# Kernel optimization log

Hardware: AMD Instinct MI355X
Metric: run time of the kernel (lower is better)

## Reference

```python
import jax, jax.numpy as jnp
import numpy as np

KH, KW = 3, 3
PAD, STRIDE, DIL, GROUPS = 1, 1, 1, 1
KK = KH * KW


def setup_inputs() -> dict:
    key = jax.random.key(0)
    ks = jax.random.split(key, 5)
    B, Cin, H, W = 8, 256, 64, 64
    Cout = 256
    x = jax.random.normal(ks[0], (B, Cin, H, W), jnp.float32)
    # offset conv: Conv2d(Cin -> 2*KK, 3x3, pad 1), small init so offsets are modest
    w_off = jax.random.normal(ks[1], (2 * KK, Cin, KH, KW), jnp.float32) * 0.01
    b_off = jax.random.normal(ks[2], (2 * KK,), jnp.float32) * 0.01
    # deformable conv weights: [Cout, Cin/groups, KH, KW]
    w_dcn = jax.random.normal(ks[3], (Cout, Cin // GROUPS, KH, KW), jnp.float32) * 0.05
    b_dcn = jax.random.normal(ks[4], (Cout,), jnp.float32) * 0.05
    return {"x": x, "w_off": w_off, "b_off": b_off, "w_dcn": w_dcn, "b_dcn": b_dcn}


def _deform_conv2d(x, offsets, w, b):
    """Deformable conv v1 (torchvision semantics, zero padding outside image).
    x: [B,Cin,Hin,Win], offsets: [B,2*KK,Ho,Wo] with (dy,dx) interleaved per tap.
    """
    B, Cin, Hin, Win = x.shape
    Ho, Wo = offsets.shape[2], offsets.shape[3]
    Cout = w.shape[0]

    off = offsets.reshape(B, KK, 2, Ho, Wo)
    off_y, off_x = off[:, :, 0], off[:, :, 1]  # [B,KK,Ho,Wo]

    # base sampling grid per kernel tap k = kh*KW + kw
    base_ky = (jnp.repeat(jnp.arange(KH), KW) * DIL).astype(jnp.float32)  # [KK]
    base_kx = (jnp.tile(jnp.arange(KW), KH) * DIL).astype(jnp.float32)
    hs = (jnp.arange(Ho) * STRIDE - PAD).astype(jnp.float32)
    ws = (jnp.arange(Wo) * STRIDE - PAD).astype(jnp.float32)

    py = hs[None, None, :, None] + base_ky[None, :, None, None] + off_y  # [B,KK,Ho,Wo]
    px = ws[None, None, None, :] + base_kx[None, :, None, None] + off_x

    iy0f = jnp.floor(py)
    ix0f = jnp.floor(px)
    fy = py - iy0f
    fx = px - ix0f
    iy0 = iy0f.astype(jnp.int32)
    ix0 = ix0f.astype(jnp.int32)

    x_flat = x.reshape(B, Cin, Hin * Win)

    def gather(iy, ix, wgt):
        valid = (iy >= 0) & (iy < Hin) & (ix >= 0) & (ix < Win)
        idx = (jnp.clip(iy, 0, Hin - 1) * Win + jnp.clip(ix, 0, Win - 1)).reshape(B, -1)
        vals = jnp.take_along_axis(x_flat, idx[:, None, :], axis=2)  # [B,Cin,KK*Ho*Wo]
        return vals * (wgt * valid).reshape(B, 1, -1)

    samp = (gather(iy0, ix0, (1 - fy) * (1 - fx))
            + gather(iy0, ix0 + 1, (1 - fy) * fx)
            + gather(iy0 + 1, ix0, fy * (1 - fx))
            + gather(iy0 + 1, ix0 + 1, fy * fx))  # [B,Cin,KK*Ho*Wo]

    samp = samp.reshape(B, GROUPS, Cin // GROUPS, KK, Ho, Wo)
    wg = w.reshape(GROUPS, Cout // GROUPS, Cin // GROUPS, KK)
    out = jnp.einsum('gock,bgckhw->bgohw', wg, samp).reshape(B, Cout, Ho, Wo)
    return out + b[None, :, None, None]


def reference(x, w_off, b_off, w_dcn, b_dcn):
    offsets = jax.lax.conv_general_dilated(
        x, w_off, window_strides=(STRIDE, STRIDE),
        padding=[(PAD, PAD), (PAD, PAD)], rhs_dilation=(DIL, DIL),
        dimension_numbers=('NCHW', 'OIHW', 'NCHW')) + b_off[None, :, None, None]
    return _deform_conv2d(x, offsets, w_dcn, b_dcn)
```

## Files before the change

### kernel.cpp

```cpp
#include <hip/hip_runtime.h>

#define HN 64
#define WN 64
#define HW 4096
#define CIN 256
#define COUT 256
#define NKK 9
#define OFFC 18
#define KTOT 2304
#define CICH 32
#define KCH 288
#define SROW 296
#define NCHUNK 8

typedef __attribute__((ext_vector_type(8))) short bf16x8;
typedef __attribute__((ext_vector_type(4))) float f32x4;

static __device__ __forceinline__ unsigned short f2bf(float f) {
    unsigned u = __float_as_uint(f);
    return (unsigned short)((u + 0x7FFFu + ((u >> 16) & 1u)) >> 16);
}
static __device__ __forceinline__ unsigned pk2(float a, float b) {
    return (unsigned)f2bf(a) | ((unsigned)f2bf(b) << 16);
}
static __device__ __forceinline__ float bf2f(short s) {
    return __uint_as_float(((unsigned)(unsigned short)s) << 16);
}

__global__ __launch_bounds__(256) void prep_kernel(
    const float* __restrict__ x, const float* __restrict__ w_dcn,
    const float* __restrict__ w_off, unsigned short* __restrict__ xh,
    unsigned short* __restrict__ wd_b, unsigned short* __restrict__ wo_b)
{
    const int blk = blockIdx.x;
    const int t = threadIdx.x;
    if (blk < 512) {
        __shared__ unsigned short lds[64 * 264];
        const int b = blk >> 6;
        const int row = blk & 63;
        const int p = t & 63;
        const int cb = (t >> 6) * 8;
        const float* xp = x + (size_t)b * CIN * HW + row * WN + p;
#pragma unroll
        for (int i = 0; i < 8; ++i) {
            const int c0 = cb + i * 32;
            float v[8];
#pragma unroll
            for (int j = 0; j < 8; ++j)
                v[j] = xp[(size_t)(c0 + j) * HW];
            uint4 o = { pk2(v[0],v[1]), pk2(v[2],v[3]), pk2(v[4],v[5]), pk2(v[6],v[7]) };
            *(uint4*)&lds[p * 264 + c0] = o;
        }
        __syncthreads();
        unsigned short* op = xh + ((size_t)b * HW + row * WN) * CIN;
#pragma unroll
        for (int i = 0; i < 8; ++i) {
            const int idx = i * 256 + t;
            const int cg = idx & 31, pp = idx >> 5;
            *(uint4*)(op + (size_t)pp * CIN + cg * 8) = *(const uint4*)&lds[pp * 264 + cg * 8];
        }
    } else if (blk < 768) {
        const int cout = blk - 512;
        for (int id = t; id < 288; id += 256) {
            const int k = id * 8;
            const int kk = k >> 8, c0 = k & 255;
            const float* wp = w_dcn + (size_t)cout * KTOT + kk;
            float v[8];
#pragma unroll
            for (int j = 0; j < 8; ++j) v[j] = wp[(size_t)(c0 + j) * NKK];
            uint4 o = { pk2(v[0],v[1]), pk2(v[2],v[3]), pk2(v[4],v[5]), pk2(v[6],v[7]) };
            *(uint4*)(wd_b + (size_t)cout * KTOT + k) = o;
        }
    } else {
        const int r = blk - 768;
        for (int id = t; id < 288; id += 256) {
            const int k = id * 8;
            const int kk = k >> 8, c0 = k & 255;
            uint4 o = {0u, 0u, 0u, 0u};
            if (r < OFFC) {
                const float* wp = w_off + (size_t)r * KTOT + kk;
                float v[8];
#pragma unroll
                for (int j = 0; j < 8; ++j) v[j] = wp[(size_t)(c0 + j) * NKK];
                o = (uint4){ pk2(v[0],v[1]), pk2(v[2],v[3]), pk2(v[4],v[5]), pk2(v[6],v[7]) };
            }
            *(uint4*)(wo_b + (size_t)r * KTOT + k) = o;
        }
    }
}

__global__ __launch_bounds__(256) void offs_mfma_kernel(
    const unsigned short* __restrict__ xh, const unsigned short* __restrict__ wo_b,
    const float* __restrict__ b_off, float* __restrict__ offs)
{
    __shared__ unsigned short samp[64 * SROW];
    const int blk = blockIdx.x;
    const int b = blk >> 6;
    const int tile = blk & 63;
    const int ty0 = (tile >> 3) << 3;
    const int tx0 = (tile & 7) << 3;
    const int t = threadIdx.x;
    const int lane = t & 63;
    const int wave = t >> 6;
    const unsigned short* xb = xh + (size_t)b * HW * CIN;

    f32x4 acc0 = {0.f,0.f,0.f,0.f}, acc1 = {0.f,0.f,0.f,0.f};

    for (int chunk = 0; chunk < NCHUNK; ++chunk) {
        const int ci0 = chunk * CICH;
        __syncthreads();
        for (int id = t; id < 2304; id += 256) {
            const int kk = id >> 8;
            const int px = (id >> 2) & 63;
            const int g = id & 3;
            const int ky = kk / 3;
            const int oy = ty0 + (px >> 3) + ky - 1;
            const int ox = tx0 + (px & 7) + (kk - ky * 3) - 1;
            bf16x8 v = {0,0,0,0,0,0,0,0};
            if ((unsigned)oy < HN && (unsigned)ox < WN)
                v = *(const bf16x8*)(xb + (size_t)(oy * WN + ox) * CIN + ci0 + g * 8);
            *(bf16x8*)&samp[px * SROW + kk * 32 + g * 8] = v;
        }
        __syncthreads();
        const unsigned short* wb = wo_b + (size_t)(lane & 15) * KTOT + ci0 + (lane >> 4) * 8;
        const unsigned short* sb = &samp[(wave * 16 + (lane & 15)) * SROW + (lane >> 4) * 8];
#pragma unroll
        for (int s = 0; s < 9; ++s) {
            const bf16x8 bfr = *(const bf16x8*)(sb + s * 32);
            const bf16x8 a0 = *(const bf16x8*)(wb + s * 256);
            const bf16x8 a1 = *(const bf16x8*)(wb + (size_t)16 * KTOT + s * 256);
            acc0 = __builtin_amdgcn_mfma_f32_16x16x32_bf16(a0, bfr, acc0, 0, 0, 0);
            acc1 = __builtin_amdgcn_mfma_f32_16x16x32_bf16(a1, bfr, acc1, 0, 0, 0);
        }
    }
    const int px = wave * 16 + (lane & 15);
    const int wy = ty0 + (px >> 3), wx = tx0 + (px & 7);
#pragma unroll
    for (int j = 0; j < 4; ++j) {
        const int c0 = (lane >> 4) * 4 + j;
        if (c0 < OFFC)
            offs[((size_t)b * OFFC + c0) * HW + wy * WN + wx] = acc0[j] + b_off[c0];
        const int c1 = 16 + c0;
        if (c1 < OFFC)
            offs[((size_t)b * OFFC + c1) * HW + wy * WN + wx] = acc1[j] + b_off[c1];
    }
}

__global__ __launch_bounds__(512, 4) void dcn_mfma_kernel(
    const unsigned short* __restrict__ xh, const float* __restrict__ offs,
    const unsigned short* __restrict__ wd_b, const float* __restrict__ bias,
    float* __restrict__ out)
{
    __shared__ unsigned short samp[64 * SROW];
    __shared__ uint4  tidx[576];
    __shared__ float4 twgt[576];

    const int blk = blockIdx.x;
    const int b = blk >> 6;
    const int tile = blk & 63;
    const int ty0 = (tile >> 3) << 3;
    const int tx0 = (tile & 7) << 3;
    const int t = threadIdx.x;
    const int lane = t & 63;
    const int wave = t >> 6;
    const unsigned short* xb = xh + (size_t)b * HW * CIN;

    for (int i = t; i < 576; i += 512) {
        const int kk = i >> 6, p = i & 63;
        const int oy = ty0 + (p >> 3), ox = tx0 + (p & 7);
        const float offy = offs[((size_t)b * OFFC + 2 * kk) * HW + oy * WN + ox];
        const float offx = offs[((size_t)b * OFFC + 2 * kk + 1) * HW + oy * WN + ox];
        const int ky = kk / 3;
        const float pyf = (float)(oy - 1 + ky) + offy;
        const float pxf = (float)(ox - 1 + (kk - ky * 3)) + offx;
        const float fy0 = floorf(pyf), fx0 = floorf(pxf);
        const int iy0 = (int)fy0, ix0 = (int)fx0;
        const int iy1 = iy0 + 1, ix1 = ix0 + 1;
        const float fy = pyf - fy0, fx = pxf - fx0;
        const float vy0 = ((unsigned)iy0 < HN) ? 1.f : 0.f;
        const float vy1 = ((unsigned)iy1 < HN) ? 1.f : 0.f;
        const float vx0 = ((unsigned)ix0 < WN) ? 1.f : 0.f;
        const float vx1 = ((unsigned)ix1 < WN) ? 1.f : 0.f;
        const int cy0 = min(max(iy0, 0), HN - 1), cy1 = min(max(iy1, 0), HN - 1);
        const int cx0 = min(max(ix0, 0), WN - 1), cx1 = min(max(ix1, 0), WN - 1);
        tidx[i] = make_uint4((unsigned)(cy0 * WN + cx0) * CIN, (unsigned)(cy0 * WN + cx1) * CIN,
                             (unsigned)(cy1 * WN + cx0) * CIN, (unsigned)(cy1 * WN + cx1) * CIN);
        twgt[i] = make_float4((1.f - fy) * (1.f - fx) * vy0 * vx0,
                              (1.f - fy) * fx * vy0 * vx1,
                              fy * (1.f - fx) * vy1 * vx0,
                              fy * fx * vy1 * vx1);
    }

    f32x4 acc[2][4];
#pragma unroll
    for (int i = 0; i < 2; ++i)
#pragma unroll
        for (int j = 0; j < 4; ++j) acc[i][j] = (f32x4){0.f, 0.f, 0.f, 0.f};

    for (int chunk = 0; chunk < NCHUNK; ++chunk) {
        const int ci0 = chunk * CICH;
        __syncthreads();
        for (int id = t; id < 2304; id += 512) {
            const int kk = id >> 8;
            const int px = (id >> 2) & 63;
            const int g = id & 3;
            const uint4 ti = tidx[kk * 64 + px];
            const float4 tw = twgt[kk * 64 + px];
            const unsigned short* base = xb + ci0 + g * 8;
            const bf16x8 A  = *(const bf16x8*)(base + ti.x);
            const bf16x8 Bv = *(const bf16x8*)(base + ti.y);
            const bf16x8 Cv = *(const bf16x8*)(base + ti.z);
            const bf16x8 Dv = *(const bf16x8*)(base + ti.w);
            unsigned r[4];
#pragma unroll
            for (int q = 0; q < 4; ++q) {
                const float v0 = tw.x * bf2f(A[2*q])   + tw.y * bf2f(Bv[2*q])
                               + tw.z * bf2f(Cv[2*q])  + tw.w * bf2f(Dv[2*q]);
                const float v1 = tw.x * bf2f(A[2*q+1]) + tw.y * bf2f(Bv[2*q+1])
                               + tw.z * bf2f(Cv[2*q+1])+ tw.w * bf2f(Dv[2*q+1]);
                r[q] = pk2(v0, v1);
            }
            *(uint4*)&samp[px * SROW + kk * 32 + g * 8] = (uint4){r[0], r[1], r[2], r[3]};
        }
        __syncthreads();
        const unsigned short* wb = wd_b + (size_t)(wave * 32 + (lane & 15)) * KTOT + ci0 + (lane >> 4) * 8;
        const unsigned short* sb = &samp[(lane & 15) * SROW + (lane >> 4) * 8];
#pragma unroll
        for (int s = 0; s < 9; ++s) {
            bf16x8 afr[2], bfr[4];
            afr[0] = *(const bf16x8*)(wb + s * 256);
            afr[1] = *(const bf16x8*)(wb + (size_t)16 * KTOT + s * 256);
#pragma unroll
            for (int pt = 0; pt < 4; ++pt)
                bfr[pt] = *(const bf16x8*)(sb + pt * 16 * SROW + s * 32);
#pragma unroll
            for (int ct = 0; ct < 2; ++ct)
#pragma unroll
                for (int pt = 0; pt < 4; ++pt)
                    acc[ct][pt] = __builtin_amdgcn_mfma_f32_16x16x32_bf16(afr[ct], bfr[pt], acc[ct][pt], 0, 0, 0);
        }
    }

#pragma unroll
    for (int ct = 0; ct < 2; ++ct) {
#pragma unroll
        for (int pt = 0; pt < 4; ++pt) {
            const int px = pt * 16 + (lane & 15);
            const int wy = ty0 + (px >> 3), wx = tx0 + (px & 7);
#pragma unroll
            for (int j = 0; j < 4; ++j) {
                const int cout = wave * 32 + ct * 16 + (lane >> 4) * 4 + j;
                out[((size_t)b * COUT + cout) * HW + wy * WN + wx] = acc[ct][pt][j] + bias[cout];
            }
        }
    }
}

extern "C" void kernel_launch(void* const* d_in, const int* in_sizes, int n_in,
                              void* d_out, int out_size, void* d_ws, size_t ws_size,
                              hipStream_t stream) {
    const float* x     = (const float*)d_in[0];
    const float* w_off = (const float*)d_in[1];
    const float* b_off = (const float*)d_in[2];
    const float* w_dcn = (const float*)d_in[3];
    const float* b_dcn = (const float*)d_in[4];
    float* out = (float*)d_out;

    float* offs          = (float*)d_ws;
    unsigned short* wd_b = (unsigned short*)((char*)d_ws + 2359296);
    unsigned short* wo_b = (unsigned short*)((char*)d_ws + 2359296 + 1179648);
    unsigned short* xh   = (unsigned short*)((char*)d_ws + 2359296 + 1179648 + 147456);

    prep_kernel<<<800, 256, 0, stream>>>(x, w_dcn, w_off, xh, wd_b, wo_b);
    offs_mfma_kernel<<<512, 256, 0, stream>>>(xh, wo_b, b_off, offs);
    dcn_mfma_kernel<<<512, 512, 0, stream>>>(xh, offs, wd_b, b_dcn, out);
}
```

Measured before the change: 235.4 us.

## Drop LDS staging in offset conv, widen DCN blocks to 1024 threads

The offset-conv kernel stops staging im2col tiles in shared memory. Each lane now loads its bf16 fragments straight from global memory, which removes the barriers and LDS traffic. The deformable conv kernel moves to 1024-thread blocks, so each wave owns 16 output channels instead of 32. This halves per-wave accumulators and spreads the bilinear sampling across more threads. Block-to-(batch, tile) mapping is interleaved across batches, and the sampling loads are split to reduce register pressure, at the cost of fewer MFMAs per A-fragment and redundant global reads in the offset kernel.

```diff
diff --git a/kernel.cpp b/kernel.cpp
--- a/kernel.cpp
+++ b/kernel.cpp
@@ -93,48 +93,40 @@
     const unsigned short* __restrict__ xh, const unsigned short* __restrict__ wo_b,
     const float* __restrict__ b_off, float* __restrict__ offs)
 {
-    __shared__ unsigned short samp[64 * SROW];
     const int blk = blockIdx.x;
-    const int b = blk >> 6;
-    const int tile = blk & 63;
+    const int b = blk & 7;
+    const int tile = blk >> 3;
     const int ty0 = (tile >> 3) << 3;
     const int tx0 = (tile & 7) << 3;
     const int t = threadIdx.x;
     const int lane = t & 63;
     const int wave = t >> 6;
-    const unsigned short* xb = xh + (size_t)b * HW * CIN;
+    const int pxl = wave * 16 + (lane & 15);
+    const int kq8 = (lane >> 4) * 8;
+    const int oy = ty0 + (pxl >> 3);
+    const int ox = tx0 + (pxl & 7);
+    const unsigned short* xb = xh + (size_t)b * HW * CIN + kq8;
+    const unsigned short* wrow = wo_b + (size_t)(lane & 15) * KTOT + kq8;
 
     f32x4 acc0 = {0.f,0.f,0.f,0.f}, acc1 = {0.f,0.f,0.f,0.f};
-
-    for (int chunk = 0; chunk < NCHUNK; ++chunk) {
-        const int ci0 = chunk * CICH;
-        __syncthreads();
-        for (int id = t; id < 2304; id += 256) {
-            const int kk = id >> 8;
-            const int px = (id >> 2) & 63;
-            const int g = id & 3;
-            const int ky = kk / 3;
-            const int oy = ty0 + (px >> 3) + ky - 1;
-            const int ox = tx0 + (px & 7) + (kk - ky * 3) - 1;
-            bf16x8 v = {0,0,0,0,0,0,0,0};
-            if ((unsigned)oy < HN && (unsigned)ox < WN)
-                v = *(const bf16x8*)(xb + (size_t)(oy * WN + ox) * CIN + ci0 + g * 8);
-            *(bf16x8*)&samp[px * SROW + kk * 32 + g * 8] = v;
-        }
-        __syncthreads();
-        const unsigned short* wb = wo_b + (size_t)(lane & 15) * KTOT + ci0 + (lane >> 4) * 8;
-        const unsigned short* sb = &samp[(wave * 16 + (lane & 15)) * SROW + (lane >> 4) * 8];
-#pragma unroll
-        for (int s = 0; s < 9; ++s) {
-            const bf16x8 bfr = *(const bf16x8*)(sb + s * 32);
-            const bf16x8 a0 = *(const bf16x8*)(wb + s * 256);
-            const bf16x8 a1 = *(const bf16x8*)(wb + (size_t)16 * KTOT + s * 256);
+#pragma unroll
+    for (int kk = 0; kk < 9; ++kk) {
+        const int yy = oy + kk / 3 - 1;
+        const int xx = ox + kk % 3 - 1;
+        const bool valid = ((unsigned)yy < HN) && ((unsigned)xx < WN);
+        const unsigned short* bp = xb + (size_t)(yy * WN + xx) * CIN;
+        const unsigned short* wp = wrow + kk * 256;
+#pragma unroll
+        for (int s = 0; s < 8; ++s) {
+            const bf16x8 bfr = valid ? *(const bf16x8*)(bp + s * 32)
+                                     : (bf16x8){0,0,0,0,0,0,0,0};
+            const bf16x8 a0 = *(const bf16x8*)(wp + s * 32);
+            const bf16x8 a1 = *(const bf16x8*)(wp + (size_t)16 * KTOT + s * 32);
             acc0 = __builtin_amdgcn_mfma_f32_16x16x32_bf16(a0, bfr, acc0, 0, 0, 0);
             acc1 = __builtin_amdgcn_mfma_f32_16x16x32_bf16(a1, bfr, acc1, 0, 0, 0);
         }
     }
-    const int px = wave * 16 + (lane & 15);
-    const int wy = ty0 + (px >> 3), wx = tx0 + (px & 7);
+    const int wy = ty0 + (pxl >> 3), wx = tx0 + (pxl & 7);
 #pragma unroll
     for (int j = 0; j < 4; ++j) {
         const int c0 = (lane >> 4) * 4 + j;
@@ -146,7 +138,31 @@
     }
 }
 
-__global__ __launch_bounds__(512, 4) void dcn_mfma_kernel(
+static __device__ __forceinline__ void sample_one(
+    int id, const unsigned short* __restrict__ xb, int ci0,
+    const uint4* __restrict__ tidx, const float4* __restrict__ twgt,
+    unsigned short* __restrict__ samp)
+{
+    const int kk = id >> 8;
+    const int px = (id >> 2) & 63;
+    const int g  = id & 3;
+    const uint4  ti = tidx[kk * 64 + px];
+    const float4 tw = twgt[kk * 64 + px];
+    const unsigned short* base = xb + ci0 + g * 8;
+    const bf16x8 A  = *(const bf16x8*)(base + ti.x);
+    const bf16x8 Bv = *(const bf16x8*)(base + ti.y);
+    float v[8];
+#pragma unroll
+    for (int e = 0; e < 8; ++e) v[e] = tw.x * bf2f(A[e]) + tw.y * bf2f(Bv[e]);
+    const bf16x8 Cv = *(const bf16x8*)(base + ti.z);
+    const bf16x8 Dv = *(const bf16x8*)(base + ti.w);
+#pragma unroll
+    for (int e = 0; e < 8; ++e) v[e] += tw.z * bf2f(Cv[e]) + tw.w * bf2f(Dv[e]);
+    uint4 o = { pk2(v[0],v[1]), pk2(v[2],v[3]), pk2(v[4],v[5]), pk2(v[6],v[7]) };
+    *(uint4*)&samp[px * SROW + kk * 32 + g * 8] = o;
+}
+
+__global__ __launch_bounds__(1024, 8) void dcn_mfma_kernel(
     const unsigned short* __restrict__ xh, const float* __restrict__ offs,
     const unsigned short* __restrict__ wd_b, const float* __restrict__ bias,
     float* __restrict__ out)
@@ -156,8 +172,8 @@
     __shared__ float4 twgt[576];
 
     const int blk = blockIdx.x;
-    const int b = blk >> 6;
-    const int tile = blk & 63;
+    const int b = blk & 7;
+    const int tile = blk >> 3;
     const int ty0 = (tile >> 3) << 3;
     const int tx0 = (tile & 7) << 3;
     const int t = threadIdx.x;
@@ -165,7 +181,7 @@
     const int wave = t >> 6;
     const unsigned short* xb = xh + (size_t)b * HW * CIN;
 
-    for (int i = t; i < 576; i += 512) {
+    for (int i = t; i < 576; i += 1024) {
         const int kk = i >> 6, p = i & 63;
         const int oy = ty0 + (p >> 3), ox = tx0 + (p & 7);
         const float offy = offs[((size_t)b * OFFC + 2 * kk) * HW + oy * WN + ox];
@@ -191,68 +207,46 @@
                               fy * fx * vy1 * vx1);
     }
 
-    f32x4 acc[2][4];
-#pragma unroll
-    for (int i = 0; i < 2; ++i)
-#pragma unroll
-        for (int j = 0; j < 4; ++j) acc[i][j] = (f32x4){0.f, 0.f, 0.f, 0.f};
+    f32x4 acc0 = {0.f,0.f,0.f,0.f}, acc1 = {0.f,0.f,0.f,0.f};
+    f32x4 acc2 = {0.f,0.f,0.f,0.f}, acc3 = {0.f,0.f,0.f,0.f};
 
     for (int chunk = 0; chunk < NCHUNK; ++chunk) {
         const int ci0 = chunk * CICH;
         __syncthreads();
-        for (int id = t; id < 2304; id += 512) {
-            const int kk = id >> 8;
-            const int px = (id >> 2) & 63;
-            const int g = id & 3;
-            const uint4 ti = tidx[kk * 64 + px];
-            const float4 tw = twgt[kk * 64 + px];
-            const unsigned short* base = xb + ci0 + g * 8;
-            const bf16x8 A  = *(const bf16x8*)(base + ti.x);
-            const bf16x8 Bv = *(const bf16x8*)(base + ti.y);
-            const bf16x8 Cv = *(const bf16x8*)(base + ti.z);
-            const bf16x8 Dv = *(const bf16x8*)(base + ti.w);
-            unsigned r[4];
-#pragma unroll
-            for (int q = 0; q < 4; ++q) {
-                const float v0 = tw.x * bf2f(A[2*q])   + tw.y * bf2f(Bv[2*q])
-                               + tw.z * bf2f(Cv[2*q])  + tw.w * bf2f(Dv[2*q]);
-                const float v1 = tw.x * bf2f(A[2*q+1]) + tw.y * bf2f(Bv[2*q+1])
-                               + tw.z * bf2f(Cv[2*q+1])+ tw.w * bf2f(Dv[2*q+1]);
-                r[q] = pk2(v0, v1);
-            }
-            *(uint4*)&samp[px * SROW + kk * 32 + g * 8] = (uint4){r[0], r[1], r[2], r[3]};
-        }
+        sample_one(t,        xb, ci0, tidx, twgt, samp);
+        sample_one(t + 1024, xb, ci0, tidx, twgt, samp);
+        if (t < 256) sample_one(t + 2048, xb, ci0, tidx, twgt, samp);
         __syncthreads();
-        const unsigned short* wb = wd_b + (size_t)(wave * 32 + (lane & 15)) * KTOT + ci0 + (lane >> 4) * 8;
+        const unsigned short* wb = wd_b + (size_t)(wave * 16 + (lane & 15)) * KTOT
+                                 + ci0 + (lane >> 4) * 8;
         const unsigned short* sb = &samp[(lane & 15) * SROW + (lane >> 4) * 8];
 #pragma unroll
         for (int s = 0; s < 9; ++s) {
-            bf16x8 afr[2], bfr[4];
-            afr[0] = *(const bf16x8*)(wb + s * 256);
-            afr[1] = *(const bf16x8*)(wb + (size_t)16 * KTOT + s * 256);
-#pragma unroll
-            for (int pt = 0; pt < 4; ++pt)
-                bfr[pt] = *(const bf16x8*)(sb + pt * 16 * SROW + s * 32);
-#pragma unroll
-            for (int ct = 0; ct < 2; ++ct)
-#pragma unroll
-                for (int pt = 0; pt < 4; ++pt)
-                    acc[ct][pt] = __builtin_amdgcn_mfma_f32_16x16x32_bf16(afr[ct], bfr[pt], acc[ct][pt], 0, 0, 0);
-        }
-    }
-
-#pragma unroll
-    for (int ct = 0; ct < 2; ++ct) {
-#pragma unroll
-        for (int pt = 0; pt < 4; ++pt) {
-            const int px = pt * 16 + (lane & 15);
-            const int wy = ty0 + (px >> 3), wx = tx0 + (px & 7);
-#pragma unroll
-            for (int j = 0; j < 4; ++j) {
-                const int cout = wave * 32 + ct * 16 + (lane >> 4) * 4 + j;
-                out[((size_t)b * COUT + cout) * HW + wy * WN + wx] = acc[ct][pt][j] + bias[cout];
-            }
-        }
+            const bf16x8 a    = *(const bf16x8*)(wb + s * 256);
+            const bf16x8 bfr0 = *(const bf16x8*)(sb + s * 32);
+            const bf16x8 bfr1 = *(const bf16x8*)(sb + 16 * SROW + s * 32);
+            const bf16x8 bfr2 = *(const bf16x8*)(sb + 32 * SROW + s * 32);
+            const bf16x8 bfr3 = *(const bf16x8*)(sb + 48 * SROW + s * 32);
+            acc0 = __builtin_amdgcn_mfma_f32_16x16x32_bf16(a, bfr0, acc0, 0, 0, 0);
+            acc1 = __builtin_amdgcn_mfma_f32_16x16x32_bf16(a, bfr1, acc1, 0, 0, 0);
+            acc2 = __builtin_amdgcn_mfma_f32_16x16x32_bf16(a, bfr2, acc2, 0, 0, 0);
+            acc3 = __builtin_amdgcn_mfma_f32_16x16x32_bf16(a, bfr3, acc3, 0, 0, 0);
+        }
+    }
+
+    const int row4 = (lane >> 4) * 4;
+    float bv[4];
+#pragma unroll
+    for (int j = 0; j < 4; ++j) bv[j] = bias[wave * 16 + row4 + j];
+    const f32x4 av[4] = {acc0, acc1, acc2, acc3};
+#pragma unroll
+    for (int pt = 0; pt < 4; ++pt) {
+        const int px = pt * 16 + (lane & 15);
+        const int wy = ty0 + (px >> 3), wx = tx0 + (px & 7);
+        float* op = out + ((size_t)b * COUT + wave * 16 + row4) * HW + wy * WN + wx;
+#pragma unroll
+        for (int j = 0; j < 4; ++j)
+            op[(size_t)j * HW] = av[pt][j] + bv[j];
     }
 }
 
@@ -273,5 +267,5 @@
 
     prep_kernel<<<800, 256, 0, stream>>>(x, w_dcn, w_off, xh, wd_b, wo_b);
     offs_mfma_kernel<<<512, 256, 0, stream>>>(xh, wo_b, b_off, offs);
-    dcn_mfma_kernel<<<512, 512, 0, stream>>>(xh, offs, wd_b, b_dcn, out);
-}
+    dcn_mfma_kernel<<<512, 1024, 0, stream>>>(xh, offs, wd_b, b_dcn, out);
+}
```

After: 234.6 us. No clear change (-0.4%).
